# Performance work log

Measured on AMD Instinct MI355X. Metric: run time of the kernel, lower is better.

The kernel has to match this reference:

```python
import jax, jax.numpy as jnp
import numpy as np

L, D, DFF, H, B, S = 6, 1024, 4096, 16, 4, 512
DK = D // H
EPS = 1e-6


def setup_inputs() -> dict:
    key = jax.random.key(0)
    ks = jax.random.split(key, 20)
    sc = 0.02
    n = jax.random.normal
    return {
        "x": n(ks[0], (B, S, D), jnp.float32),
        "Wq": n(ks[1], (L, D, D)) * sc, "bq": jnp.zeros((L, D)),
        "Wk": n(ks[2], (L, D, D)) * sc, "bk": jnp.zeros((L, D)),
        "Wv": n(ks[3], (L, D, D)) * sc, "bv": jnp.zeros((L, D)),
        "Wo": n(ks[4], (L, D, D)) * sc, "bo": jnp.zeros((L, D)),
        "W1": n(ks[5], (L, D, DFF)) * sc, "b1": jnp.zeros((L, DFF)),
        "W2": n(ks[6], (L, DFF, D)) * sc, "b2": jnp.zeros((L, D)),
        "ln1_a": jnp.ones((L, D)), "ln1_b": jnp.zeros((L, D)),
        "ln2_a": jnp.ones((L, D)), "ln2_b": jnp.zeros((L, D)),
        "norm_a": jnp.ones((D,)), "norm_b": jnp.zeros((D,)),
    }


def _ln(x, a, b):
    # custom LayerNorm: uses sample std (ddof=1, like torch.std) and (std + eps)
    m = x.mean(-1, keepdims=True)
    s = jnp.std(x, axis=-1, ddof=1, keepdims=True)
    return a * (x - m) / (s + EPS) + b


def reference(x, Wq, bq, Wk, bk, Wv, bv, Wo, bo, W1, b1, W2, b2,
              ln1_a, ln1_b, ln2_a, ln2_b, norm_a, norm_b):
    inv = 1.0 / jnp.sqrt(jnp.float32(DK))
    for l in range(L):
        # --- self-attention sublayer (pre-norm, residual) ---
        h = _ln(x, ln1_a[l], ln1_b[l])
        q = (h @ Wq[l] + bq[l]).reshape(B, S, H, DK)
        k = (h @ Wk[l] + bk[l]).reshape(B, S, H, DK)
        v = (h @ Wv[l] + bv[l]).reshape(B, S, H, DK)
        scores = jnp.einsum('bqhd,bkhd->bhqk', q, k) * inv
        p = jax.nn.softmax(scores, axis=-1)
        o = jnp.einsum('bhqk,bkhd->bqhd', p, v).reshape(B, S, D)
        x = x + (o @ Wo[l] + bo[l])
        # --- feed-forward sublayer ---
        h = _ln(x, ln2_a[l], ln2_b[l])
        x = x + (jax.nn.relu(h @ W1[l] + b1[l]) @ W2[l] + b2[l])
    return _ln(x, norm_a, norm_b)
```

## Files before the change

kernel.cpp:

```cpp
#include <hip/hip_runtime.h>
#include <hip/hip_bf16.h>

typedef __hip_bfloat16 bf16;
typedef __bf16 bf16x8 __attribute__((ext_vector_type(8)));
typedef float f32x4 __attribute__((ext_vector_type(4)));

static constexpr int L_ = 6, D_ = 1024, DFF_ = 4096, H_ = 16, B_ = 4, S_ = 512, DK_ = 64;
static constexpr int N_ = B_ * S_;

#define GLOAD_LDS(gp, lp) __builtin_amdgcn_global_load_lds( \
    (const __attribute__((address_space(1))) void*)(gp),    \
    (__attribute__((address_space(3))) void*)(lp), 16, 0, 0)

__global__ void transpose_cast(const float* __restrict__ in, bf16* __restrict__ out,
                               int K, int M, long zin, long zout) {
    const float* ip = in + (size_t)blockIdx.z * zin;
    bf16* op = out + (size_t)blockIdx.z * zout;
    __shared__ float t[32][33];
    int m0 = blockIdx.x * 32, k0 = blockIdx.y * 32;
    int tx = threadIdx.x, ty = threadIdx.y;
    #pragma unroll
    for (int i = 0; i < 32; i += 8)
        t[ty + i][tx] = ip[(size_t)(k0 + ty + i) * M + m0 + tx];
    __syncthreads();
    #pragma unroll
    for (int i = 0; i < 32; i += 8)
        op[(size_t)(m0 + ty + i) * K + k0 + tx] = __float2bfloat16(t[tx][ty + i]);
}

__global__ void pack_qkv_bias(const float* __restrict__ bq, const float* __restrict__ bk,
                              const float* __restrict__ bv, float* __restrict__ out) {
    int t = blockIdx.x * 256 + threadIdx.x;
    int l = t / (3 * D_), c = t % (3 * D_);
    float v = c < D_ ? bq[l * D_ + c] : (c < 2 * D_ ? bk[l * D_ + c - D_] : bv[l * D_ + c - 2 * D_]);
    out[t] = v;
}

template <typename OutT>
__global__ __launch_bounds__(256) void ln_kernel(const float* __restrict__ x,
                                                 const float* __restrict__ ga,
                                                 const float* __restrict__ gb,
                                                 OutT* __restrict__ out) {
    int row = blockIdx.x;
    float4 v = ((const float4*)(x + (size_t)row * D_))[threadIdx.x];
    float s = v.x + v.y + v.z + v.w;
    float q = v.x * v.x + v.y * v.y + v.z * v.z + v.w * v.w;
    #pragma unroll
    for (int m = 1; m < 64; m <<= 1) { s += __shfl_xor(s, m, 64); q += __shfl_xor(q, m, 64); }
    __shared__ float ps[4], pq[4];
    int wid = threadIdx.x >> 6;
    if ((threadIdx.x & 63) == 0) { ps[wid] = s; pq[wid] = q; }
    __syncthreads();
    s = ps[0] + ps[1] + ps[2] + ps[3];
    q = pq[0] + pq[1] + pq[2] + pq[3];
    float mean = s * (1.0f / D_);
    float var = (q - (float)D_ * mean * mean) * (1.0f / (D_ - 1));
    var = var < 0.f ? 0.f : var;
    float rstd = 1.0f / (sqrtf(var) + 1e-6f);
    int c = threadIdx.x * 4;
    float xv[4] = {v.x, v.y, v.z, v.w};
    #pragma unroll
    for (int r = 0; r < 4; r++) {
        float o = ga[c + r] * (xv[r] - mean) * rstd + gb[c + r];
        if constexpr (__hip_internal::is_same<OutT, float>::value)
            out[(size_t)row * D_ + c + r] = o;
        else
            out[(size_t)row * D_ + c + r] = __float2bfloat16(o);
    }
}

template <int S, typename OutT>
__global__ __launch_bounds__(256) void reduce_ln(
    const float* __restrict__ parts, long sK, float* __restrict__ xf,
    const float* __restrict__ ga, const float* __restrict__ gb, OutT* __restrict__ out) {
    int row = blockIdx.x;
    float4 v = ((const float4*)(xf + (size_t)row * D_))[threadIdx.x];
    #pragma unroll
    for (int s = 0; s < S; s++) {
        float4 p = ((const float4*)(parts + (size_t)s * sK + (size_t)row * D_))[threadIdx.x];
        v.x += p.x; v.y += p.y; v.z += p.z; v.w += p.w;
    }
    ((float4*)(xf + (size_t)row * D_))[threadIdx.x] = v;
    float sum = v.x + v.y + v.z + v.w;
    float q = v.x * v.x + v.y * v.y + v.z * v.z + v.w * v.w;
    #pragma unroll
    for (int m = 1; m < 64; m <<= 1) { sum += __shfl_xor(sum, m, 64); q += __shfl_xor(q, m, 64); }
    __shared__ float ps[4], pq[4];
    int wid = threadIdx.x >> 6;
    if ((threadIdx.x & 63) == 0) { ps[wid] = sum; pq[wid] = q; }
    __syncthreads();
    sum = ps[0] + ps[1] + ps[2] + ps[3];
    q = pq[0] + pq[1] + pq[2] + pq[3];
    float mean = sum * (1.0f / D_);
    float var = (q - (float)D_ * mean * mean) * (1.0f / (D_ - 1));
    var = var < 0.f ? 0.f : var;
    float rstd = 1.0f / (sqrtf(var) + 1e-6f);
    int c = threadIdx.x * 4;
    float xv[4] = {v.x, v.y, v.z, v.w};
    #pragma unroll
    for (int r = 0; r < 4; r++) {
        float o = ga[c + r] * (xv[r] - mean) * rstd + gb[c + r];
        if constexpr (__hip_internal::is_same<OutT, float>::value)
            out[(size_t)row * D_ + c + r] = o;
        else
            out[(size_t)row * D_ + c + r] = __float2bfloat16(o);
    }
}

__device__ inline void swz_tiles(int& ntile, int& mtile) {
    unsigned o = blockIdx.y * gridDim.x + blockIdx.x;
    if (gridDim.z == 1 && (gridDim.x & 7) == 0) {
        unsigned xcd = o & 7, j = o >> 3;
        unsigned cn = gridDim.x >> 3;
        ntile = xcd * cn + j / gridDim.y;
        mtile = j % gridDim.y;
    } else {
        ntile = o % gridDim.x;
        mtile = o / gridDim.x;
    }
}

enum { EPI_RELU = 0, EPI_PART = 1, EPI_QKV = 2 };

template <int EPI, int SPLITK = 1>
__global__ __launch_bounds__(256) void gemm4(
    const bf16* __restrict__ A, int lda,
    const bf16* __restrict__ Bt, int ldb,
    const float* __restrict__ bias,
    void* __restrict__ Cv, int ldc, long sK, int K,
    bf16* __restrict__ qb, bf16* __restrict__ kb, bf16* __restrict__ vT) {
    constexpr int BM = 128, BN = 128, BK = 64;
    constexpr int FM = 4, FN = 4;
    constexpr int IA = BM / 32;
    constexpr int IB = BN / 32;
    __shared__ __align__(16) bf16 As[BM * BK];
    __shared__ __align__(16) bf16 Bs[BN * BK];
    const int tid = threadIdx.x, wid = tid >> 6, lane = tid & 63;
    const int kz = (SPLITK > 1) ? blockIdx.z : 0;
    int ntile, mtile;
    swz_tiles(ntile, mtile);
    const int m0 = mtile * BM, n0 = ntile * BN;
    const int wm = (wid >> 1) * 64, wn = (wid & 1) * 64;
    const int fr = lane & 15, fg = lane >> 4;
    const int sr = lane >> 3;
    const int c8s = (lane & 7) ^ (sr & 7);
    const int Kc = K / SPLITK;
    const int kbeg = kz * Kc, kend = kbeg + Kc;

    f32x4 acc[FM][FN] = {};
    for (int k0 = kbeg; k0 < kend; k0 += BK) {
        __syncthreads();
        #pragma unroll
        for (int i = 0; i < IA; i++) {
            int inst = wid * IA + i;
            const bf16* gp = A + (size_t)(m0 + inst * 8 + sr) * lda + k0 + c8s * 8;
            GLOAD_LDS(gp, &As[inst * 512]);
        }
        #pragma unroll
        for (int i = 0; i < IB; i++) {
            int inst = wid * IB + i;
            const bf16* gp = Bt + (size_t)(n0 + inst * 8 + sr) * ldb + k0 + c8s * 8;
            GLOAD_LDS(gp, &Bs[inst * 512]);
        }
        __syncthreads();
        #pragma unroll
        for (int kk = 0; kk < 2; kk++) {
            const int cs = ((kk << 2) + fg) ^ (fr & 7);
            bf16x8 af[FM], bfr[FN];
            #pragma unroll
            for (int i = 0; i < FM; i++)
                af[i] = *(const bf16x8*)&As[(wm + i * 16 + fr) * BK + cs * 8];
            #pragma unroll
            for (int j = 0; j < FN; j++)
                bfr[j] = *(const bf16x8*)&Bs[(wn + j * 16 + fr) * BK + cs * 8];
            #pragma unroll
            for (int i = 0; i < FM; i++)
                #pragma unroll
                for (int j = 0; j < FN; j++)
                    acc[i][j] = __builtin_amdgcn_mfma_f32_16x16x32_bf16(af[i], bfr[j], acc[i][j], 0, 0, 0);
        }
    }
    #pragma unroll
    for (int i = 0; i < FM; i++) {
        #pragma unroll
        for (int j = 0; j < FN; j++) {
            int rr = m0 + wm + i * 16 + (lane >> 4) * 4;
            int cc = n0 + wn + j * 16 + (lane & 15);
            float bv = bias[cc];
            #pragma unroll
            for (int r = 0; r < 4; r++) {
                float v = acc[i][j][r];
                if constexpr (EPI == EPI_RELU) {
                    bf16* C = (bf16*)Cv;
                    float o = v + bv;
                    C[(size_t)(rr + r) * ldc + cc] = __float2bfloat16(o > 0.f ? o : 0.f);
                } else if constexpr (EPI == EPI_PART) {
                    float* C = (float*)Cv;
                    C[(size_t)kz * sK + (size_t)(rr + r) * ldc + cc] = v + (kz == 0 ? bv : 0.f);
                } else {
                    float o = v + bv;
                    if (cc < D_) {
                        qb[(size_t)(rr + r) * D_ + cc] = __float2bfloat16(o);
                    } else if (cc < 2 * D_) {
                        kb[(size_t)(rr + r) * D_ + cc - D_] = __float2bfloat16(o);
                    } else {
                        vT[((size_t)(rr >> 9) * D_ + cc - 2 * D_) * S_ + ((rr & 511) + r)] = __float2bfloat16(o);
                    }
                }
            }
        }
    }
}

__global__ __launch_bounds__(256) void flash_attn(
    const bf16* __restrict__ qb, const bf16* __restrict__ kb, const bf16* __restrict__ vT,
    bf16* __restrict__ ob) {
    __shared__ __align__(16) bf16 P[4][16 * 64];
    const int lane = threadIdx.x & 63, wid = threadIdx.x >> 6;
    const int b = blockIdx.y >> 4, h = blockIdx.y & 15;
    const int q0 = blockIdx.x * 64 + wid * 16;
    const int fr = lane & 15, fg = lane >> 4;
    bf16* Pw = &P[wid][0];

    const bf16* qrow = qb + ((size_t)(b * S_ + q0 + fr)) * D_ + h * DK_ + fg * 8;
    bf16x8 aq0 = *(const bf16x8*)(qrow);
    bf16x8 aq1 = *(const bf16x8*)(qrow + 32);

    f32x4 accO[4] = {};
    float mrow[4] = {-1e30f, -1e30f, -1e30f, -1e30f};
    float lrow[4] = {};

    for (int kv0 = 0; kv0 < S_; kv0 += 64) {
        f32x4 s[4] = {};
        #pragma unroll
        for (int j = 0; j < 4; j++) {
            const bf16* krow = kb + ((size_t)(b * S_ + kv0 + j * 16 + fr)) * D_ + h * DK_ + fg * 8;
            bf16x8 bk0 = *(const bf16x8*)(krow);
            bf16x8 bk1 = *(const bf16x8*)(krow + 32);
            s[j] = __builtin_amdgcn_mfma_f32_16x16x32_bf16(aq0, bk0, s[j], 0, 0, 0);
            s[j] = __builtin_amdgcn_mfma_f32_16x16x32_bf16(aq1, bk1, s[j], 0, 0, 0);
        }
        float tmax[4], alpha[4], rs[4];
        #pragma unroll
        for (int r = 0; r < 4; r++) {
            #pragma unroll
            for (int j = 0; j < 4; j++) s[j][r] *= 0.125f;
            tmax[r] = fmaxf(fmaxf(s[0][r], s[1][r]), fmaxf(s[2][r], s[3][r]));
            #pragma unroll
            for (int m = 1; m < 16; m <<= 1) tmax[r] = fmaxf(tmax[r], __shfl_xor(tmax[r], m, 64));
            float mn = fmaxf(mrow[r], tmax[r]);
            alpha[r] = __expf(mrow[r] - mn);
            mrow[r] = mn;
            rs[r] = 0.f;
        }
        #pragma unroll
        for (int j = 0; j < 4; j++) {
            #pragma unroll
            for (int r = 0; r < 4; r++) {
                float p = __expf(s[j][r] - mrow[r]);
                rs[r] += p;
                int q = fg * 4 + r;
                int col = (j * 16 + fr) ^ ((q & 7) << 3);
                Pw[q * 64 + col] = __float2bfloat16(p);
            }
        }
        #pragma unroll
        for (int r = 0; r < 4; r++) {
            #pragma unroll
            for (int m = 1; m < 16; m <<= 1) rs[r] += __shfl_xor(rs[r], m, 64);
            lrow[r] = lrow[r] * alpha[r] + rs[r];
            #pragma unroll
            for (int j = 0; j < 4; j++) accO[j][r] *= alpha[r];
        }
        #pragma unroll
        for (int ks = 0; ks < 2; ks++) {
            int kk = (ks * 32 + fg * 8) ^ ((fr & 7) << 3);
            bf16x8 ap = *(const bf16x8*)&Pw[fr * 64 + kk];
            #pragma unroll
            for (int j = 0; j < 4; j++) {
                const bf16* vrow = vT + ((size_t)(b * D_) + h * DK_ + j * 16 + fr) * S_ + kv0 + ks * 32 + fg * 8;
                bf16x8 bv = *(const bf16x8*)(vrow);
                accO[j] = __builtin_amdgcn_mfma_f32_16x16x32_bf16(ap, bv, accO[j], 0, 0, 0);
            }
        }
    }
    #pragma unroll
    for (int j = 0; j < 4; j++) {
        #pragma unroll
        for (int r = 0; r < 4; r++) {
            int q = q0 + fg * 4 + r;
            int d = h * DK_ + j * 16 + fr;
            ob[(size_t)(b * S_ + q) * D_ + d] = __float2bfloat16(accO[j][r] / lrow[r]);
        }
    }
}

extern "C" void kernel_launch(void* const* d_in, const int* in_sizes, int n_in,
                              void* d_out, int out_size, void* d_ws, size_t ws_size,
                              hipStream_t stream) {
    (void)in_sizes; (void)n_in; (void)out_size;
    const float* x    = (const float*)d_in[0];
    const float* Wq   = (const float*)d_in[1];
    const float* pbq  = (const float*)d_in[2];
    const float* Wk   = (const float*)d_in[3];
    const float* pbk  = (const float*)d_in[4];
    const float* Wv   = (const float*)d_in[5];
    const float* pbv  = (const float*)d_in[6];
    const float* Wo   = (const float*)d_in[7];
    const float* pbo  = (const float*)d_in[8];
    const float* W1   = (const float*)d_in[9];
    const float* pb1  = (const float*)d_in[10];
    const float* W2   = (const float*)d_in[11];
    const float* pb2  = (const float*)d_in[12];
    const float* l1a  = (const float*)d_in[13];
    const float* l1b  = (const float*)d_in[14];
    const float* l2a  = (const float*)d_in[15];
    const float* l2b  = (const float*)d_in[16];
    const float* nrma = (const float*)d_in[17];
    const float* nrmb = (const float*)d_in[18];

    char* ws = (char*)d_ws;
    size_t off = 0;
    auto alloc = [&](size_t bytes) { void* p = ws + off; off += (bytes + 255) & ~(size_t)255; return p; };
    float* xf  = (float*)alloc((size_t)N_ * D_ * 4);
    bf16* hbuf = (bf16*)alloc((size_t)N_ * D_ * 2);
    bf16* qbuf = (bf16*)alloc((size_t)N_ * D_ * 2);
    bf16* kbuf = (bf16*)alloc((size_t)N_ * D_ * 2);
    bf16* vT   = (bf16*)alloc((size_t)B_ * D_ * S_ * 2);
    bf16* obuf = (bf16*)alloc((size_t)N_ * D_ * 2);
    float* qkvb = (float*)alloc((size_t)L_ * 3 * D_ * 4);
    bf16* mid  = (bf16*)alloc((size_t)N_ * DFF_ * 2);
    float* wsP = (float*)alloc((size_t)4 * N_ * D_ * 4);
    const size_t szDD = (size_t)D_ * D_, szDF = (size_t)D_ * DFF_;
    const long sK = (long)N_ * D_;
    size_t wtFull = (3 * L_ * szDD + L_ * szDD + 2 * L_ * szDF) * 2;
    size_t wtLayer = (4 * szDD + 2 * szDF) * 2;
    bool full = (off + wtFull) <= ws_size;
    bf16* WT = (bf16*)alloc(full ? wtFull : wtLayer);

    pack_qkv_bias<<<L_ * 3 * D_ / 256, 256, 0, stream>>>(pbq, pbk, pbv, qkvb);

    bf16 *Wqkv0, *WoT0, *W1T0, *W2T0;
    dim3 tb(32, 8);
    if (full) {
        Wqkv0 = WT;
        WoT0  = WT + 3 * L_ * szDD;
        W1T0  = WoT0 + L_ * szDD;
        W2T0  = W1T0 + L_ * szDF;
        transpose_cast<<<dim3(D_ / 32, D_ / 32, L_), tb, 0, stream>>>(Wq, Wqkv0, D_, D_, szDD, 3 * szDD);
        transpose_cast<<<dim3(D_ / 32, D_ / 32, L_), tb, 0, stream>>>(Wk, Wqkv0 + szDD, D_, D_, szDD, 3 * szDD);
        transpose_cast<<<dim3(D_ / 32, D_ / 32, L_), tb, 0, stream>>>(Wv, Wqkv0 + 2 * szDD, D_, D_, szDD, 3 * szDD);
        transpose_cast<<<dim3(D_ / 32, D_ / 32, L_), tb, 0, stream>>>(Wo, WoT0, D_, D_, szDD, szDD);
        transpose_cast<<<dim3(DFF_ / 32, D_ / 32, L_), tb, 0, stream>>>(W1, W1T0, D_, DFF_, szDF, szDF);
        transpose_cast<<<dim3(D_ / 32, DFF_ / 32, L_), tb, 0, stream>>>(W2, W2T0, DFF_, D_, szDF, szDF);
    } else {
        Wqkv0 = WT; WoT0 = WT + 3 * szDD; W1T0 = WoT0 + szDD; W2T0 = W1T0 + szDF;
    }

    hipMemcpyAsync(xf, x, (size_t)N_ * D_ * 4, hipMemcpyDeviceToDevice, stream);
    ln_kernel<bf16><<<N_, 256, 0, stream>>>(xf, l1a, l1b, hbuf);

    for (int l = 0; l < L_; l++) {
        const bf16 *WqkvT, *WoT, *W1T, *W2T;
        if (full) {
            WqkvT = Wqkv0 + (size_t)l * 3 * szDD;
            WoT = WoT0 + l * szDD; W1T = W1T0 + l * szDF; W2T = W2T0 + l * szDF;
        } else {
            transpose_cast<<<dim3(D_ / 32, D_ / 32, 1), tb, 0, stream>>>(Wq + l * szDD, Wqkv0, D_, D_, 0, 0);
            transpose_cast<<<dim3(D_ / 32, D_ / 32, 1), tb, 0, stream>>>(Wk + l * szDD, Wqkv0 + szDD, D_, D_, 0, 0);
            transpose_cast<<<dim3(D_ / 32, D_ / 32, 1), tb, 0, stream>>>(Wv + l * szDD, Wqkv0 + 2 * szDD, D_, D_, 0, 0);
            transpose_cast<<<dim3(D_ / 32, D_ / 32, 1), tb, 0, stream>>>(Wo + l * szDD, WoT0, D_, D_, 0, 0);
            transpose_cast<<<dim3(DFF_ / 32, D_ / 32, 1), tb, 0, stream>>>(W1 + l * szDF, W1T0, D_, DFF_, 0, 0);
            transpose_cast<<<dim3(D_ / 32, DFF_ / 32, 1), tb, 0, stream>>>(W2 + l * szDF, W2T0, DFF_, D_, 0, 0);
            WqkvT = Wqkv0; WoT = WoT0; W1T = W1T0; W2T = W2T0;
        }

        gemm4<EPI_QKV><<<dim3(3 * D_ / 128, N_ / 128, 1), 256, 0, stream>>>(
            hbuf, D_, WqkvT, D_, qkvb + (size_t)l * 3 * D_, nullptr, 0, 0, D_, qbuf, kbuf, vT);
        flash_attn<<<dim3(S_ / 64, B_ * H_), 256, 0, stream>>>(qbuf, kbuf, vT, obuf);
        gemm4<EPI_PART, 2><<<dim3(D_ / 128, N_ / 128, 2), 256, 0, stream>>>(
            obuf, D_, WoT, D_, pbo + l * D_, wsP, D_, sK, D_, nullptr, nullptr, nullptr);
        reduce_ln<2, bf16><<<N_, 256, 0, stream>>>(wsP, sK, xf, l2a + l * D_, l2b + l * D_, hbuf);
        gemm4<EPI_RELU><<<dim3(DFF_ / 128, N_ / 128, 1), 256, 0, stream>>>(
            hbuf, D_, W1T, D_, pb1 + l * DFF_, mid, DFF_, 0, D_, nullptr, nullptr, nullptr);
        gemm4<EPI_PART, 4><<<dim3(D_ / 128, N_ / 128, 4), 256, 0, stream>>>(
            mid, DFF_, W2T, DFF_, pb2 + l * D_, wsP, D_, sK, DFF_, nullptr, nullptr, nullptr);
        if (l < L_ - 1)
            reduce_ln<4, bf16><<<N_, 256, 0, stream>>>(wsP, sK, xf, l1a + (l + 1) * D_, l1b + (l + 1) * D_, hbuf);
        else
            reduce_ln<4, float><<<N_, 256, 0, stream>>>(wsP, sK, xf, nrma, nrmb, (float*)d_out);
    }
}
```

Baseline: 1.130 ms.

## Replace LDS-staged GEMM with register-direct double-buffered global loads

The GEMM kernel no longer stages A and B tiles through shared memory with global_load_lds and barriers. Each wave now loads its MFMA fragments straight from global memory into registers and double-buffers them across two 32-wide k-steps to overlap loads with MFMA work. This removes LDS traffic and __syncthreads, but the two waves that share rows or columns each fetch the same data, which doubles global/L2 traffic and leaves latency hiding to register prefetch alone.

```diff
diff --git a/kernel.cpp b/kernel.cpp
--- a/kernel.cpp
+++ b/kernel.cpp
@@ -7,10 +7,6 @@
 
 static constexpr int L_ = 6, D_ = 1024, DFF_ = 4096, H_ = 16, B_ = 4, S_ = 512, DK_ = 64;
 static constexpr int N_ = B_ * S_;
-
-#define GLOAD_LDS(gp, lp) __builtin_amdgcn_global_load_lds( \
-    (const __attribute__((address_space(1))) void*)(gp),    \
-    (__attribute__((address_space(3))) void*)(lp), 16, 0, 0)
 
 __global__ void transpose_cast(const float* __restrict__ in, bf16* __restrict__ out,
                                int K, int M, long zin, long zout) {
@@ -123,67 +119,65 @@
 enum { EPI_RELU = 0, EPI_PART = 1, EPI_QKV = 2 };
 
 template <int EPI, int SPLITK = 1>
-__global__ __launch_bounds__(256) void gemm4(
+__global__ __launch_bounds__(256) void gemmR(
     const bf16* __restrict__ A, int lda,
     const bf16* __restrict__ Bt, int ldb,
     const float* __restrict__ bias,
     void* __restrict__ Cv, int ldc, long sK, int K,
     bf16* __restrict__ qb, bf16* __restrict__ kb, bf16* __restrict__ vT) {
-    constexpr int BM = 128, BN = 128, BK = 64;
-    constexpr int FM = 4, FN = 4;
-    constexpr int IA = BM / 32;
-    constexpr int IB = BN / 32;
-    __shared__ __align__(16) bf16 As[BM * BK];
-    __shared__ __align__(16) bf16 Bs[BN * BK];
     const int tid = threadIdx.x, wid = tid >> 6, lane = tid & 63;
     const int kz = (SPLITK > 1) ? blockIdx.z : 0;
     int ntile, mtile;
     swz_tiles(ntile, mtile);
-    const int m0 = mtile * BM, n0 = ntile * BN;
+    const int m0 = mtile * 128, n0 = ntile * 128;
     const int wm = (wid >> 1) * 64, wn = (wid & 1) * 64;
     const int fr = lane & 15, fg = lane >> 4;
-    const int sr = lane >> 3;
-    const int c8s = (lane & 7) ^ (sr & 7);
     const int Kc = K / SPLITK;
     const int kbeg = kz * Kc, kend = kbeg + Kc;
 
-    f32x4 acc[FM][FN] = {};
-    for (int k0 = kbeg; k0 < kend; k0 += BK) {
-        __syncthreads();
-        #pragma unroll
-        for (int i = 0; i < IA; i++) {
-            int inst = wid * IA + i;
-            const bf16* gp = A + (size_t)(m0 + inst * 8 + sr) * lda + k0 + c8s * 8;
-            GLOAD_LDS(gp, &As[inst * 512]);
-        }
-        #pragma unroll
-        for (int i = 0; i < IB; i++) {
-            int inst = wid * IB + i;
-            const bf16* gp = Bt + (size_t)(n0 + inst * 8 + sr) * ldb + k0 + c8s * 8;
-            GLOAD_LDS(gp, &Bs[inst * 512]);
-        }
-        __syncthreads();
-        #pragma unroll
-        for (int kk = 0; kk < 2; kk++) {
-            const int cs = ((kk << 2) + fg) ^ (fr & 7);
-            bf16x8 af[FM], bfr[FN];
-            #pragma unroll
-            for (int i = 0; i < FM; i++)
-                af[i] = *(const bf16x8*)&As[(wm + i * 16 + fr) * BK + cs * 8];
-            #pragma unroll
-            for (int j = 0; j < FN; j++)
-                bfr[j] = *(const bf16x8*)&Bs[(wn + j * 16 + fr) * BK + cs * 8];
-            #pragma unroll
-            for (int i = 0; i < FM; i++)
+    const bf16* Arow = A + (size_t)(m0 + wm + fr) * lda + fg * 8;
+    const bf16* Brow = Bt + (size_t)(n0 + wn + fr) * ldb + fg * 8;
+
+    f32x4 acc[4][4] = {};
+    bf16x8 a0[4], b0[4], a1[4], b1[4];
+
+    #pragma unroll
+    for (int i = 0; i < 4; i++) {
+        a0[i] = *(const bf16x8*)(Arow + (size_t)i * 16 * lda + kbeg);
+        b0[i] = *(const bf16x8*)(Brow + (size_t)i * 16 * ldb + kbeg);
+    }
+    for (int k0 = kbeg; k0 < kend; k0 += 64) {
+        if (k0 + 32 < kend) {
+            #pragma unroll
+            for (int i = 0; i < 4; i++) {
+                a1[i] = *(const bf16x8*)(Arow + (size_t)i * 16 * lda + k0 + 32);
+                b1[i] = *(const bf16x8*)(Brow + (size_t)i * 16 * ldb + k0 + 32);
+            }
+        }
+        #pragma unroll
+        for (int i = 0; i < 4; i++)
+            #pragma unroll
+            for (int j = 0; j < 4; j++)
+                acc[i][j] = __builtin_amdgcn_mfma_f32_16x16x32_bf16(a0[i], b0[j], acc[i][j], 0, 0, 0);
+        if (k0 + 64 < kend) {
+            #pragma unroll
+            for (int i = 0; i < 4; i++) {
+                a0[i] = *(const bf16x8*)(Arow + (size_t)i * 16 * lda + k0 + 64);
+                b0[i] = *(const bf16x8*)(Brow + (size_t)i * 16 * ldb + k0 + 64);
+            }
+        }
+        if (k0 + 32 < kend) {
+            #pragma unroll
+            for (int i = 0; i < 4; i++)
                 #pragma unroll
-                for (int j = 0; j < FN; j++)
-                    acc[i][j] = __builtin_amdgcn_mfma_f32_16x16x32_bf16(af[i], bfr[j], acc[i][j], 0, 0, 0);
-        }
-    }
-    #pragma unroll
-    for (int i = 0; i < FM; i++) {
-        #pragma unroll
-        for (int j = 0; j < FN; j++) {
+                for (int j = 0; j < 4; j++)
+                    acc[i][j] = __builtin_amdgcn_mfma_f32_16x16x32_bf16(a1[i], b1[j], acc[i][j], 0, 0, 0);
+        }
+    }
+    #pragma unroll
+    for (int i = 0; i < 4; i++) {
+        #pragma unroll
+        for (int j = 0; j < 4; j++) {
             int rr = m0 + wm + i * 16 + (lane >> 4) * 4;
             int cc = n0 + wn + j * 16 + (lane & 15);
             float bv = bias[cc];
@@ -375,15 +369,15 @@
             WqkvT = Wqkv0; WoT = WoT0; W1T = W1T0; W2T = W2T0;
         }
 
-        gemm4<EPI_QKV><<<dim3(3 * D_ / 128, N_ / 128, 1), 256, 0, stream>>>(
+        gemmR<EPI_QKV><<<dim3(3 * D_ / 128, N_ / 128, 1), 256, 0, stream>>>(
             hbuf, D_, WqkvT, D_, qkvb + (size_t)l * 3 * D_, nullptr, 0, 0, D_, qbuf, kbuf, vT);
         flash_attn<<<dim3(S_ / 64, B_ * H_), 256, 0, stream>>>(qbuf, kbuf, vT, obuf);
-        gemm4<EPI_PART, 2><<<dim3(D_ / 128, N_ / 128, 2), 256, 0, stream>>>(
+        gemmR<EPI_PART, 2><<<dim3(D_ / 128, N_ / 128, 2), 256, 0, stream>>>(
             obuf, D_, WoT, D_, pbo + l * D_, wsP, D_, sK, D_, nullptr, nullptr, nullptr);
         reduce_ln<2, bf16><<<N_, 256, 0, stream>>>(wsP, sK, xf, l2a + l * D_, l2b + l * D_, hbuf);
-        gemm4<EPI_RELU><<<dim3(DFF_ / 128, N_ / 128, 1), 256, 0, stream>>>(
+        gemmR<EPI_RELU><<<dim3(DFF_ / 128, N_ / 128, 1), 256, 0, stream>>>(
             hbuf, D_, W1T, D_, pb1 + l * DFF_, mid, DFF_, 0, D_, nullptr, nullptr, nullptr);
-        gemm4<EPI_PART, 4><<<dim3(D_ / 128, N_ / 128, 4), 256, 0, stream>>>(
+        gemmR<EPI_PART, 4><<<dim3(D_ / 128, N_ / 128, 4), 256, 0, stream>>>(
             mid, DFF_, W2T, DFF_, pb2 + l * D_, wsP, D_, sK, DFF_, nullptr, nullptr, nullptr);
         if (l < L_ - 1)
             reduce_ln<4, bf16><<<N_, 256, 0, stream>>>(wsP, sK, xf, l1a + (l + 1) * D_, l1b + (l + 1) * D_, hbuf);
```

Measured after the change: 1.748 ms. 1.55x slower.
